# Kernel tuning notes

Hardware: AMD Instinct MI355X
Metric: run time of the kernel (lower is better)

The kernel has to match this reference:

```python
import jax, jax.numpy as jnp
import numpy as np

N = 50000
E = 625000
D_IN = 128
D_OUT = 128


def setup_inputs() -> dict:
    key = jax.random.key(0)
    k1, k2, k3, k4 = jax.random.split(key, 4)
    x = jax.random.normal(k1, (N, D_IN), dtype=jnp.float32)
    edge_index = jax.random.randint(k2, (2, E), 0, N, dtype=jnp.int64)
    edge_weight = jax.random.uniform(k3, (E,), dtype=jnp.float32)
    # xavier_uniform with gain=0.05: limit = gain * sqrt(6/(fan_in+fan_out))
    limit = 0.05 * np.sqrt(6.0 / (D_IN + D_OUT))
    weight = jax.random.uniform(k4, (D_OUT, D_IN), dtype=jnp.float32,
                                minval=-limit, maxval=limit)
    bias = jnp.zeros((D_OUT,), dtype=jnp.float32)
    return {"x": x, "edge_index": edge_index, "edge_weight": edge_weight,
            "weight": weight, "bias": bias}


def reference(x, edge_index, edge_weight, weight, bias):
    src = edge_index[0]
    dst = edge_index[1]
    # gather source features and weight per edge: [E, D_IN]
    msg = x[src] * edge_weight[:, None]
    # scatter-add into destination nodes: [N, D_IN]
    agg = jax.ops.segment_sum(msg, dst, num_segments=x.shape[0])
    # linear + bias + relu
    h = agg @ weight.T + bias
    return jax.nn.relu(h)
```

## Files before the change

kernel.cpp:

```cpp
#include <hip/hip_runtime.h>
#include <hip/hip_fp16.h>

#define NN 50000
#define NE 625000
#define D  128
#define CAP 64
#define NBIN 196
#define BCAP 4096
#define BIN_BLOCKS 200
#define BIN_CHUNK 3125
#define GBM 128
#define PREP_BLKS 3125

typedef __attribute__((ext_vector_type(8))) short bf16x8;
typedef __attribute__((ext_vector_type(4))) float f32x4;

__device__ inline unsigned f2bf_rne(float f) {
    unsigned u = __float_as_uint(f);
    u += 0x7FFFu + ((u >> 16) & 1u);
    return u >> 16;
}

__device__ inline unsigned pack_hi(float a, float b, float& ra, float& rb) {
    unsigned ba = __float_as_uint(a) & 0xffff0000u;
    unsigned bb = __float_as_uint(b) & 0xffff0000u;
    ra = a - __uint_as_float(ba);
    rb = b - __uint_as_float(bb);
    return (ba >> 16) | bb;
}
__device__ inline unsigned pack_lo(float ra, float rb) {
    return (__float_as_uint(ra) >> 16) | (__float_as_uint(rb) & 0xffff0000u);
}

__global__ __launch_bounds__(256) void prep(const float* __restrict__ x,
                                            const float* __restrict__ W,
                                            unsigned* __restrict__ xb,
                                            ushort* __restrict__ wsp,
                                            int* __restrict__ binc,
                                            int* __restrict__ ovf_cnt) {
    if (blockIdx.x >= PREP_BLKS) {
        int g = (blockIdx.x - PREP_BLKS) * 256 + threadIdx.x;
        if (g >= 128 * 16) return;
        int col = g >> 4;
        int c16 = g & 15;
        const float4* wp = (const float4*)(W + (size_t)col * D + c16 * 8);
        float4 v0 = wp[0], v1 = wp[1];
        float r0, r1, r2, r3, r4, r5, r6, r7;
        uint4 hi, lo;
        hi.x = pack_hi(v0.x, v0.y, r0, r1);
        hi.y = pack_hi(v0.z, v0.w, r2, r3);
        hi.z = pack_hi(v1.x, v1.y, r4, r5);
        hi.w = pack_hi(v1.z, v1.w, r6, r7);
        lo.x = pack_lo(r0, r1); lo.y = pack_lo(r2, r3);
        lo.z = pack_lo(r4, r5); lo.w = pack_lo(r6, r7);
        int sidx = col * 16 + (c16 ^ (col & 15));
        ((uint4*)wsp)[sidx] = hi;
        ((uint4*)(wsp + 16384))[sidx] = lo;
        return;
    }
    int g = blockIdx.x * 256 + threadIdx.x;
    if (g < NBIN) binc[g] = 0;
    if (g == 0) *ovf_cnt = 0;
    const float4* xp = (const float4*)(x + (size_t)g * 8);
    float4 a = xp[0], b = xp[1];
    uint4 o;
    o.x = f2bf_rne(a.x) | (f2bf_rne(a.y) << 16);
    o.y = f2bf_rne(a.z) | (f2bf_rne(a.w) << 16);
    o.z = f2bf_rne(b.x) | (f2bf_rne(b.y) << 16);
    o.w = f2bf_rne(b.z) | (f2bf_rne(b.w) << 16);
    ((uint4*)xb)[g] = o;
}

__global__ __launch_bounds__(256) void bin_coarse(const int* __restrict__ src,
                                                  const int* __restrict__ dst,
                                                  const float* __restrict__ ew,
                                                  int* __restrict__ binc,
                                                  uint2* __restrict__ binbuf,
                                                  int* __restrict__ ovf_cnt,
                                                  uint2* __restrict__ ovf) {
    __shared__ int hcnt[NBIN];
    __shared__ int hbase[NBIN];
    __shared__ int hcur[NBIN];
    const int tid = threadIdx.x;
    const int e0 = blockIdx.x * BIN_CHUNK;
    const int e1 = min(e0 + BIN_CHUNK, NE);

    for (int i = tid; i < NBIN; i += 256) hcnt[i] = 0;
    __syncthreads();
    for (int e = e0 + tid; e < e1; e += 256)
        atomicAdd(&hcnt[dst[e] >> 8], 1);
    __syncthreads();
    for (int i = tid; i < NBIN; i += 256) {
        int c = hcnt[i];
        hbase[i] = c ? atomicAdd(&binc[i], c) : 0;
        hcur[i] = 0;
    }
    __syncthreads();
    for (int e = e0 + tid; e < e1; e += 256) {
        int d = dst[e];
        int bin = d >> 8;
        unsigned entry = ((unsigned)src[e] << 16) |
                         (unsigned)__half_as_ushort(__float2half(ew[e]));
        int slot = hbase[bin] + atomicAdd(&hcur[bin], 1);
        if (slot < BCAP) {
            binbuf[(size_t)bin * BCAP + slot] = make_uint2((unsigned)d, entry);
        } else {
            int o = atomicAdd(ovf_cnt, 1);
            ovf[o] = make_uint2((unsigned)d, entry);
        }
    }
}

__global__ __launch_bounds__(256) void bin_fill(const int* __restrict__ binc,
                                                const uint2* __restrict__ binbuf,
                                                int* __restrict__ fillc,
                                                unsigned* __restrict__ buck,
                                                int* __restrict__ ovf_cnt,
                                                uint2* __restrict__ ovf) {
    __shared__ int lcnt[256];
    const int tid = threadIdx.x;
    const int bin = blockIdx.x;
    lcnt[tid] = 0;
    __syncthreads();
    int n = binc[bin];
    if (n > BCAP) n = BCAP;
    const uint2* bp = binbuf + (size_t)bin * BCAP;
    for (int i = tid; i < n; i += 256) {
        uint2 q = bp[i];
        int d = (int)q.x;
        int p = atomicAdd(&lcnt[d & 255], 1);
        if (p < CAP) {
            buck[(size_t)d * CAP + p] = q.y;
        } else {
            int o = atomicAdd(ovf_cnt, 1);
            ovf[o] = q;
        }
    }
    __syncthreads();
    int node = bin * 256 + tid;
    if (node < NN) fillc[node] = lcnt[tid];
}

__global__ __launch_bounds__(256) void aggregate(const unsigned* __restrict__ xb,
                                                 const int* __restrict__ fillc,
                                                 const unsigned* __restrict__ buck,
                                                 float* __restrict__ agg) {
    int node = blockIdx.x * 4 + (threadIdx.x >> 6);
    int t    = threadIdx.x & 63;
    if (node >= NN) return;
    int cnt = fillc[node];
    if (cnt > CAP) cnt = CAP;
    const unsigned* bp = buck + (size_t)node * CAP;
    float2 acc{0.f, 0.f};
    int i = 0;
    for (; i + 3 < cnt; i += 4) {
        unsigned q0 = bp[i], q1 = bp[i + 1], q2 = bp[i + 2], q3 = bp[i + 3];
        unsigned u0 = xb[(size_t)(q0 >> 16) * 64 + t];
        unsigned u1 = xb[(size_t)(q1 >> 16) * 64 + t];
        unsigned u2 = xb[(size_t)(q2 >> 16) * 64 + t];
        unsigned u3 = xb[(size_t)(q3 >> 16) * 64 + t];
        float w0 = __half2float(__ushort_as_half((ushort)(q0 & 0xffffu)));
        float w1 = __half2float(__ushort_as_half((ushort)(q1 & 0xffffu)));
        float w2 = __half2float(__ushort_as_half((ushort)(q2 & 0xffffu)));
        float w3 = __half2float(__ushort_as_half((ushort)(q3 & 0xffffu)));
        acc.x += __uint_as_float(u0 << 16) * w0;
        acc.y += __uint_as_float(u0 & 0xffff0000u) * w0;
        acc.x += __uint_as_float(u1 << 16) * w1;
        acc.y += __uint_as_float(u1 & 0xffff0000u) * w1;
        acc.x += __uint_as_float(u2 << 16) * w2;
        acc.y += __uint_as_float(u2 & 0xffff0000u) * w2;
        acc.x += __uint_as_float(u3 << 16) * w3;
        acc.y += __uint_as_float(u3 & 0xffff0000u) * w3;
    }
    for (; i < cnt; ++i) {
        unsigned q0 = bp[i];
        unsigned u0 = xb[(size_t)(q0 >> 16) * 64 + t];
        float w0 = __half2float(__ushort_as_half((ushort)(q0 & 0xffffu)));
        acc.x += __uint_as_float(u0 << 16) * w0;
        acc.y += __uint_as_float(u0 & 0xffff0000u) * w0;
    }
    reinterpret_cast<float2*>(agg)[(size_t)node * 64 + t] = acc;
}

__global__ __launch_bounds__(256) void ovf_fix(const unsigned* __restrict__ xb,
                                               const int* __restrict__ ovf_cnt,
                                               const uint2* __restrict__ ovf,
                                               float* __restrict__ agg) {
    int n = *ovf_cnt;
    int widx = (blockIdx.x * 256 + threadIdx.x) >> 6;
    int t = threadIdx.x & 63;
    int nw = gridDim.x * 4;
    for (int o = widx; o < n; o += nw) {
        unsigned d = ovf[o].x;
        unsigned q = ovf[o].y;
        unsigned u = xb[(size_t)(q >> 16) * 64 + t];
        float w = __half2float(__ushort_as_half((ushort)(q & 0xffffu)));
        atomicAdd(&agg[(size_t)d * D + 2 * t],     __uint_as_float(u << 16) * w);
        atomicAdd(&agg[(size_t)d * D + 2 * t + 1], __uint_as_float(u & 0xffff0000u) * w);
    }
}

__global__ __launch_bounds__(256) void gemm_mfma(const float* __restrict__ agg,
                                                 const ushort* __restrict__ wsp,
                                                 const float* __restrict__ bias,
                                                 float* __restrict__ out) {
    __shared__ ushort wl[32768];
    const int tid = threadIdx.x;
    {
        const uint4* s = (const uint4*)wsp;
        uint4* d = (uint4*)wl;
#pragma unroll
        for (int i = 0; i < 16; ++i)
            d[i * 256 + tid] = s[i * 256 + tid];
    }
    __syncthreads();

    const int wid = tid >> 6, lane = tid & 63;
    const int l15 = lane & 15, kg = lane >> 4;
    const int wrbase = blockIdx.x * GBM + wid * 32;

    f32x4 acc[2][8];
    const f32x4 fz = {0.f, 0.f, 0.f, 0.f};
#pragma unroll
    for (int m = 0; m < 2; ++m)
#pragma unroll
        for (int n = 0; n < 8; ++n) acc[m][n] = fz;

    int arow0 = wrbase + l15;
    int arow1 = wrbase + 16 + l15;
    const float* a0p = agg + (size_t)(arow0 < NN ? arow0 : NN - 1) * D + kg * 8;
    const float* a1p = agg + (size_t)(arow1 < NN ? arow1 : NN - 1) * D + kg * 8;

#pragma unroll
    for (int kk = 0; kk < 4; ++kk) {
        float4 u0 = *(const float4*)(a0p + kk * 32);
        float4 u1 = *(const float4*)(a0p + kk * 32 + 4);
        float4 v0 = *(const float4*)(a1p + kk * 32);
        float4 v1 = *(const float4*)(a1p + kk * 32 + 4);
        float r0, r1, r2, r3, r4, r5, r6, r7;
        uint4 h0, l0, h1, l1;
        h0.x = pack_hi(u0.x, u0.y, r0, r1);
        h0.y = pack_hi(u0.z, u0.w, r2, r3);
        h0.z = pack_hi(u1.x, u1.y, r4, r5);
        h0.w = pack_hi(u1.z, u1.w, r6, r7);
        l0.x = pack_lo(r0, r1); l0.y = pack_lo(r2, r3);
        l0.z = pack_lo(r4, r5); l0.w = pack_lo(r6, r7);
        h1.x = pack_hi(v0.x, v0.y, r0, r1);
        h1.y = pack_hi(v0.z, v0.w, r2, r3);
        h1.z = pack_hi(v1.x, v1.y, r4, r5);
        h1.w = pack_hi(v1.z, v1.w, r6, r7);
        l1.x = pack_lo(r0, r1); l1.y = pack_lo(r2, r3);
        l1.z = pack_lo(r4, r5); l1.w = pack_lo(r6, r7);
        bf16x8 a0hi = *(bf16x8*)&h0;
        bf16x8 a0lo = *(bf16x8*)&l0;
        bf16x8 a1hi = *(bf16x8*)&h1;
        bf16x8 a1lo = *(bf16x8*)&l1;

        int coff = ((kk * 4 + kg) ^ l15) * 8;
#pragma unroll
        for (int nf = 0; nf < 8; ++nf) {
            int bidx = (16 * nf + l15) * 128 + coff;
            bf16x8 bhi = *(const bf16x8*)&wl[bidx];
            bf16x8 blo = *(const bf16x8*)&wl[16384 + bidx];
            acc[0][nf] = __builtin_amdgcn_mfma_f32_16x16x32_bf16(a0hi, bhi, acc[0][nf], 0, 0, 0);
            acc[1][nf] = __builtin_amdgcn_mfma_f32_16x16x32_bf16(a1hi, bhi, acc[1][nf], 0, 0, 0);
            acc[0][nf] = __builtin_amdgcn_mfma_f32_16x16x32_bf16(a0lo, bhi, acc[0][nf], 0, 0, 0);
            acc[1][nf] = __builtin_amdgcn_mfma_f32_16x16x32_bf16(a1lo, bhi, acc[1][nf], 0, 0, 0);
            acc[0][nf] = __builtin_amdgcn_mfma_f32_16x16x32_bf16(a0hi, blo, acc[0][nf], 0, 0, 0);
            acc[1][nf] = __builtin_amdgcn_mfma_f32_16x16x32_bf16(a1hi, blo, acc[1][nf], 0, 0, 0);
        }
    }

    const int rofs = kg * 4;
#pragma unroll
    for (int nf = 0; nf < 8; ++nf) {
        int col = 16 * nf + l15;
        float bv = bias[col];
#pragma unroll
        for (int m = 0; m < 2; ++m) {
#pragma unroll
            for (int r = 0; r < 4; ++r) {
                int row = wrbase + 16 * m + rofs + r;
                if (row < NN) {
                    float h = acc[m][nf][r] + bv;
                    out[(size_t)row * D + col] = h > 0.f ? h : 0.f;
                }
            }
        }
    }
}

extern "C" void kernel_launch(void* const* d_in, const int* in_sizes, int n_in,
                              void* d_out, int out_size, void* d_ws, size_t ws_size,
                              hipStream_t stream) {
    const float* x    = (const float*)d_in[0];
    const int*   eidx = (const int*)d_in[1];
    const float* ew   = (const float*)d_in[2];
    const float* W    = (const float*)d_in[3];
    const float* bias = (const float*)d_in[4];
    float* out = (float*)d_out;

    const int* src = eidx;
    const int* dst = eidx + NE;

    char* base = (char*)d_ws;
    float*    agg    = (float*)base;
    uint2*    binbuf = (uint2*)base;
    unsigned* buck   = (unsigned*)(base + 25600000);
    unsigned* xb     = (unsigned*)(base + 25600000 + 12800000);
    ushort*   wsp    = (ushort*)(base + 51200000);
    int*      fillc   = (int*)(base + 51200000 + 65536);
    int*      binc    = (int*)(base + 51200000 + 65536 + 200000);
    int*      ovf_cnt = (int*)(base + 51200000 + 65536 + 200000 + 1024);
    uint2*    ovf     = (uint2*)(base + 51200000 + 65536 + 200000 + 1024 + 16);

    prep<<<PREP_BLKS + 8, 256, 0, stream>>>(x, W, xb, wsp, binc, ovf_cnt);
    bin_coarse<<<BIN_BLOCKS, 256, 0, stream>>>(src, dst, ew, binc, binbuf, ovf_cnt, ovf);
    bin_fill<<<NBIN, 256, 0, stream>>>(binc, binbuf, fillc, buck, ovf_cnt, ovf);
    aggregate<<<(NN + 3) / 4, 256, 0, stream>>>(xb, fillc, buck, agg);
    ovf_fix<<<8, 256, 0, stream>>>(xb, ovf_cnt, ovf, agg);
    gemm_mfma<<<(NN + GBM - 1) / GBM, 256, 0, stream>>>(agg, wsp, bias, out);
}
```

Baseline: 87.49 us.

## Fuse prep with coarse binning, fold overflow into aggregate, widen gather

Merges the bf16 conversion, weight split and coarse edge binning into one launch, with binc and ovf_cnt zeroed by a memset beforehand. The coarse histogram now uses one copy per wave to cut shared-memory atomic contention. Aggregation moves to half-wave per node with 8-byte gathers, and overflow edges are handled inside aggregate by a linear scan of the overflow list, removing the separate atomic fix-up kernel. This saves two launches and the atomics, but every node now scans the whole overflow list, which costs a lot if overflow is large. The aggregate also drops its node<NN check and relies on the grid being exact.

```diff
diff --git a/kernel.cpp b/kernel.cpp
--- a/kernel.cpp
+++ b/kernel.cpp
@@ -11,6 +11,9 @@
 #define BIN_CHUNK 3125
 #define GBM 128
 #define PREP_BLKS 3125
+#define MEGA_X  BIN_BLOCKS
+#define MEGA_W  (BIN_BLOCKS + PREP_BLKS)
+#define MEGA_GRID (MEGA_W + 8)
 
 typedef __attribute__((ext_vector_type(8))) short bf16x8;
 typedef __attribute__((ext_vector_type(4))) float f32x4;
@@ -32,83 +35,82 @@
     return (__float_as_uint(ra) >> 16) | (__float_as_uint(rb) & 0xffff0000u);
 }
 
-__global__ __launch_bounds__(256) void prep(const float* __restrict__ x,
-                                            const float* __restrict__ W,
-                                            unsigned* __restrict__ xb,
-                                            ushort* __restrict__ wsp,
-                                            int* __restrict__ binc,
-                                            int* __restrict__ ovf_cnt) {
-    if (blockIdx.x >= PREP_BLKS) {
-        int g = (blockIdx.x - PREP_BLKS) * 256 + threadIdx.x;
-        if (g >= 128 * 16) return;
-        int col = g >> 4;
-        int c16 = g & 15;
-        const float4* wp = (const float4*)(W + (size_t)col * D + c16 * 8);
-        float4 v0 = wp[0], v1 = wp[1];
-        float r0, r1, r2, r3, r4, r5, r6, r7;
-        uint4 hi, lo;
-        hi.x = pack_hi(v0.x, v0.y, r0, r1);
-        hi.y = pack_hi(v0.z, v0.w, r2, r3);
-        hi.z = pack_hi(v1.x, v1.y, r4, r5);
-        hi.w = pack_hi(v1.z, v1.w, r6, r7);
-        lo.x = pack_lo(r0, r1); lo.y = pack_lo(r2, r3);
-        lo.z = pack_lo(r4, r5); lo.w = pack_lo(r6, r7);
-        int sidx = col * 16 + (c16 ^ (col & 15));
-        ((uint4*)wsp)[sidx] = hi;
-        ((uint4*)(wsp + 16384))[sidx] = lo;
+__global__ __launch_bounds__(256) void mega1(const float* __restrict__ x,
+                                             const float* __restrict__ W,
+                                             const int* __restrict__ src,
+                                             const int* __restrict__ dst,
+                                             const float* __restrict__ ew,
+                                             unsigned* __restrict__ xb,
+                                             ushort* __restrict__ wsp,
+                                             int* __restrict__ binc,
+                                             uint2* __restrict__ binbuf,
+                                             int* __restrict__ ovf_cnt,
+                                             uint2* __restrict__ ovf) {
+    const int tid = threadIdx.x;
+    if (blockIdx.x < MEGA_X) {
+        __shared__ int hcnt[4][NBIN];
+        __shared__ int hbase[NBIN];
+        __shared__ int hcur[NBIN];
+        const int wv = tid >> 6;
+        const int e0 = blockIdx.x * BIN_CHUNK;
+        const int e1 = min(e0 + BIN_CHUNK, NE);
+        for (int i = tid; i < NBIN; i += 256) {
+            hcnt[0][i] = 0; hcnt[1][i] = 0; hcnt[2][i] = 0; hcnt[3][i] = 0;
+        }
+        __syncthreads();
+        for (int e = e0 + tid; e < e1; e += 256)
+            atomicAdd(&hcnt[wv][dst[e] >> 8], 1);
+        __syncthreads();
+        for (int i = tid; i < NBIN; i += 256) {
+            int c = hcnt[0][i] + hcnt[1][i] + hcnt[2][i] + hcnt[3][i];
+            hbase[i] = c ? atomicAdd(&binc[i], c) : 0;
+            hcur[i] = 0;
+        }
+        __syncthreads();
+        for (int e = e0 + tid; e < e1; e += 256) {
+            int d = dst[e];
+            int bin = d >> 8;
+            unsigned entry = ((unsigned)src[e] << 16) |
+                             (unsigned)__half_as_ushort(__float2half(ew[e]));
+            int slot = hbase[bin] + atomicAdd(&hcur[bin], 1);
+            if (slot < BCAP) {
+                binbuf[(size_t)bin * BCAP + slot] = make_uint2((unsigned)d, entry);
+            } else {
+                int o = atomicAdd(ovf_cnt, 1);
+                ovf[o] = make_uint2((unsigned)d, entry);
+            }
+        }
         return;
     }
-    int g = blockIdx.x * 256 + threadIdx.x;
-    if (g < NBIN) binc[g] = 0;
-    if (g == 0) *ovf_cnt = 0;
-    const float4* xp = (const float4*)(x + (size_t)g * 8);
-    float4 a = xp[0], b = xp[1];
-    uint4 o;
-    o.x = f2bf_rne(a.x) | (f2bf_rne(a.y) << 16);
-    o.y = f2bf_rne(a.z) | (f2bf_rne(a.w) << 16);
-    o.z = f2bf_rne(b.x) | (f2bf_rne(b.y) << 16);
-    o.w = f2bf_rne(b.z) | (f2bf_rne(b.w) << 16);
-    ((uint4*)xb)[g] = o;
-}
-
-__global__ __launch_bounds__(256) void bin_coarse(const int* __restrict__ src,
-                                                  const int* __restrict__ dst,
-                                                  const float* __restrict__ ew,
-                                                  int* __restrict__ binc,
-                                                  uint2* __restrict__ binbuf,
-                                                  int* __restrict__ ovf_cnt,
-                                                  uint2* __restrict__ ovf) {
-    __shared__ int hcnt[NBIN];
-    __shared__ int hbase[NBIN];
-    __shared__ int hcur[NBIN];
-    const int tid = threadIdx.x;
-    const int e0 = blockIdx.x * BIN_CHUNK;
-    const int e1 = min(e0 + BIN_CHUNK, NE);
-
-    for (int i = tid; i < NBIN; i += 256) hcnt[i] = 0;
-    __syncthreads();
-    for (int e = e0 + tid; e < e1; e += 256)
-        atomicAdd(&hcnt[dst[e] >> 8], 1);
-    __syncthreads();
-    for (int i = tid; i < NBIN; i += 256) {
-        int c = hcnt[i];
-        hbase[i] = c ? atomicAdd(&binc[i], c) : 0;
-        hcur[i] = 0;
-    }
-    __syncthreads();
-    for (int e = e0 + tid; e < e1; e += 256) {
-        int d = dst[e];
-        int bin = d >> 8;
-        unsigned entry = ((unsigned)src[e] << 16) |
-                         (unsigned)__half_as_ushort(__float2half(ew[e]));
-        int slot = hbase[bin] + atomicAdd(&hcur[bin], 1);
-        if (slot < BCAP) {
-            binbuf[(size_t)bin * BCAP + slot] = make_uint2((unsigned)d, entry);
-        } else {
-            int o = atomicAdd(ovf_cnt, 1);
-            ovf[o] = make_uint2((unsigned)d, entry);
-        }
-    }
+    if (blockIdx.x < MEGA_W) {
+        int g = (blockIdx.x - MEGA_X) * 256 + tid;
+        const float4* xp = (const float4*)(x + (size_t)g * 8);
+        float4 a = xp[0], b = xp[1];
+        uint4 o;
+        o.x = f2bf_rne(a.x) | (f2bf_rne(a.y) << 16);
+        o.y = f2bf_rne(a.z) | (f2bf_rne(a.w) << 16);
+        o.z = f2bf_rne(b.x) | (f2bf_rne(b.y) << 16);
+        o.w = f2bf_rne(b.z) | (f2bf_rne(b.w) << 16);
+        ((uint4*)xb)[g] = o;
+        return;
+    }
+    int g = (blockIdx.x - MEGA_W) * 256 + tid;
+    if (g >= 128 * 16) return;
+    int col = g >> 4;
+    int c16 = g & 15;
+    const float4* wp = (const float4*)(W + (size_t)col * D + c16 * 8);
+    float4 v0 = wp[0], v1 = wp[1];
+    float r0, r1, r2, r3, r4, r5, r6, r7;
+    uint4 hi, lo;
+    hi.x = pack_hi(v0.x, v0.y, r0, r1);
+    hi.y = pack_hi(v0.z, v0.w, r2, r3);
+    hi.z = pack_hi(v1.x, v1.y, r4, r5);
+    hi.w = pack_hi(v1.z, v1.w, r6, r7);
+    lo.x = pack_lo(r0, r1); lo.y = pack_lo(r2, r3);
+    lo.z = pack_lo(r4, r5); lo.w = pack_lo(r6, r7);
+    int sidx = col * 16 + (c16 ^ (col & 15));
+    ((uint4*)wsp)[sidx] = hi;
+    ((uint4*)(wsp + 16384))[sidx] = lo;
 }
 
 __global__ __launch_bounds__(256) void bin_fill(const int* __restrict__ binc,
@@ -144,60 +146,66 @@
 __global__ __launch_bounds__(256) void aggregate(const unsigned* __restrict__ xb,
                                                  const int* __restrict__ fillc,
                                                  const unsigned* __restrict__ buck,
+                                                 const int* __restrict__ ovf_cnt,
+                                                 const uint2* __restrict__ ovf,
                                                  float* __restrict__ agg) {
-    int node = blockIdx.x * 4 + (threadIdx.x >> 6);
-    int t    = threadIdx.x & 63;
-    if (node >= NN) return;
+    const int node = blockIdx.x * 8 + ((threadIdx.x >> 5));
+    const int t = threadIdx.x & 31;
     int cnt = fillc[node];
     if (cnt > CAP) cnt = CAP;
     const unsigned* bp = buck + (size_t)node * CAP;
-    float2 acc{0.f, 0.f};
+    const uint2* x2 = (const uint2*)xb;
+    float4 acc = {0.f, 0.f, 0.f, 0.f};
     int i = 0;
     for (; i + 3 < cnt; i += 4) {
         unsigned q0 = bp[i], q1 = bp[i + 1], q2 = bp[i + 2], q3 = bp[i + 3];
-        unsigned u0 = xb[(size_t)(q0 >> 16) * 64 + t];
-        unsigned u1 = xb[(size_t)(q1 >> 16) * 64 + t];
-        unsigned u2 = xb[(size_t)(q2 >> 16) * 64 + t];
-        unsigned u3 = xb[(size_t)(q3 >> 16) * 64 + t];
+        uint2 u0 = x2[(size_t)(q0 >> 16) * 32 + t];
+        uint2 u1 = x2[(size_t)(q1 >> 16) * 32 + t];
+        uint2 u2 = x2[(size_t)(q2 >> 16) * 32 + t];
+        uint2 u3 = x2[(size_t)(q3 >> 16) * 32 + t];
         float w0 = __half2float(__ushort_as_half((ushort)(q0 & 0xffffu)));
         float w1 = __half2float(__ushort_as_half((ushort)(q1 & 0xffffu)));
         float w2 = __half2float(__ushort_as_half((ushort)(q2 & 0xffffu)));
         float w3 = __half2float(__ushort_as_half((ushort)(q3 & 0xffffu)));
-        acc.x += __uint_as_float(u0 << 16) * w0;
-        acc.y += __uint_as_float(u0 & 0xffff0000u) * w0;
-        acc.x += __uint_as_float(u1 << 16) * w1;
-        acc.y += __uint_as_float(u1 & 0xffff0000u) * w1;
-        acc.x += __uint_as_float(u2 << 16) * w2;
-        acc.y += __uint_as_float(u2 & 0xffff0000u) * w2;
-        acc.x += __uint_as_float(u3 << 16) * w3;
-        acc.y += __uint_as_float(u3 & 0xffff0000u) * w3;
+        acc.x += __uint_as_float(u0.x << 16) * w0;
+        acc.y += __uint_as_float(u0.x & 0xffff0000u) * w0;
+        acc.z += __uint_as_float(u0.y << 16) * w0;
+        acc.w += __uint_as_float(u0.y & 0xffff0000u) * w0;
+        acc.x += __uint_as_float(u1.x << 16) * w1;
+        acc.y += __uint_as_float(u1.x & 0xffff0000u) * w1;
+        acc.z += __uint_as_float(u1.y << 16) * w1;
+        acc.w += __uint_as_float(u1.y & 0xffff0000u) * w1;
+        acc.x += __uint_as_float(u2.x << 16) * w2;
+        acc.y += __uint_as_float(u2.x & 0xffff0000u) * w2;
+        acc.z += __uint_as_float(u2.y << 16) * w2;
+        acc.w += __uint_as_float(u2.y & 0xffff0000u) * w2;
+        acc.x += __uint_as_float(u3.x << 16) * w3;
+        acc.y += __uint_as_float(u3.x & 0xffff0000u) * w3;
+        acc.z += __uint_as_float(u3.y << 16) * w3;
+        acc.w += __uint_as_float(u3.y & 0xffff0000u) * w3;
     }
     for (; i < cnt; ++i) {
         unsigned q0 = bp[i];
-        unsigned u0 = xb[(size_t)(q0 >> 16) * 64 + t];
+        uint2 u0 = x2[(size_t)(q0 >> 16) * 32 + t];
         float w0 = __half2float(__ushort_as_half((ushort)(q0 & 0xffffu)));
-        acc.x += __uint_as_float(u0 << 16) * w0;
-        acc.y += __uint_as_float(u0 & 0xffff0000u) * w0;
-    }
-    reinterpret_cast<float2*>(agg)[(size_t)node * 64 + t] = acc;
-}
-
-__global__ __launch_bounds__(256) void ovf_fix(const unsigned* __restrict__ xb,
-                                               const int* __restrict__ ovf_cnt,
-                                               const uint2* __restrict__ ovf,
-                                               float* __restrict__ agg) {
+        acc.x += __uint_as_float(u0.x << 16) * w0;
+        acc.y += __uint_as_float(u0.x & 0xffff0000u) * w0;
+        acc.z += __uint_as_float(u0.y << 16) * w0;
+        acc.w += __uint_as_float(u0.y & 0xffff0000u) * w0;
+    }
     int n = *ovf_cnt;
-    int widx = (blockIdx.x * 256 + threadIdx.x) >> 6;
-    int t = threadIdx.x & 63;
-    int nw = gridDim.x * 4;
-    for (int o = widx; o < n; o += nw) {
-        unsigned d = ovf[o].x;
-        unsigned q = ovf[o].y;
-        unsigned u = xb[(size_t)(q >> 16) * 64 + t];
-        float w = __half2float(__ushort_as_half((ushort)(q & 0xffffu)));
-        atomicAdd(&agg[(size_t)d * D + 2 * t],     __uint_as_float(u << 16) * w);
-        atomicAdd(&agg[(size_t)d * D + 2 * t + 1], __uint_as_float(u & 0xffff0000u) * w);
-    }
+    for (int o = 0; o < n; ++o) {
+        uint2 q = ovf[o];
+        if ((int)q.x == node) {
+            uint2 u = x2[(size_t)(q.y >> 16) * 32 + t];
+            float w = __half2float(__ushort_as_half((ushort)(q.y & 0xffffu)));
+            acc.x += __uint_as_float(u.x << 16) * w;
+            acc.y += __uint_as_float(u.x & 0xffff0000u) * w;
+            acc.z += __uint_as_float(u.y << 16) * w;
+            acc.w += __uint_as_float(u.y & 0xffff0000u) * w;
+        }
+    }
+    ((float4*)agg)[(size_t)node * 32 + t] = acc;
 }
 
 __global__ __launch_bounds__(256) void gemm_mfma(const float* __restrict__ agg,
@@ -311,13 +319,12 @@
     ushort*   wsp    = (ushort*)(base + 51200000);
     int*      fillc   = (int*)(base + 51200000 + 65536);
     int*      binc    = (int*)(base + 51200000 + 65536 + 200000);
-    int*      ovf_cnt = (int*)(base + 51200000 + 65536 + 200000 + 1024);
-    uint2*    ovf     = (uint2*)(base + 51200000 + 65536 + 200000 + 1024 + 16);
-
-    prep<<<PREP_BLKS + 8, 256, 0, stream>>>(x, W, xb, wsp, binc, ovf_cnt);
-    bin_coarse<<<BIN_BLOCKS, 256, 0, stream>>>(src, dst, ew, binc, binbuf, ovf_cnt, ovf);
+    int*      ovf_cnt = (int*)((char*)binc + NBIN * 4);
+    uint2*    ovf     = (uint2*)(base + 51200000 + 65536 + 200000 + 1024);
+
+    hipMemsetAsync(binc, 0, NBIN * 4 + 4, stream);
+    mega1<<<MEGA_GRID, 256, 0, stream>>>(x, W, src, dst, ew, xb, wsp, binc, binbuf, ovf_cnt, ovf);
     bin_fill<<<NBIN, 256, 0, stream>>>(binc, binbuf, fillc, buck, ovf_cnt, ovf);
-    aggregate<<<(NN + 3) / 4, 256, 0, stream>>>(xb, fillc, buck, agg);
-    ovf_fix<<<8, 256, 0, stream>>>(xb, ovf_cnt, ovf, agg);
+    aggregate<<<6250, 256, 0, stream>>>(xb, fillc, buck, ovf_cnt, ovf, agg);
     gemm_mfma<<<(NN + GBM - 1) / GBM, 256, 0, stream>>>(agg, wsp, bias, out);
 }
```

After: 85.50 us. 1.02x faster.
